# Performance work log

Hardware: AMD Instinct MI355X
Metric: run time of the kernel (lower is better)

## Reference

```python
import jax, jax.numpy as jnp
import numpy as np

B, T, N = 16, 512, 128
D, HID, S, H, L, EMB = 256, 128, 16, 512, 4, 512
EPS_BN = 1e-5
EPS_LN = 1e-5


def _ln(x, w, b):
    mu = x.mean(-1, keepdims=True)
    v = ((x - mu) ** 2).mean(-1, keepdims=True)
    return (x - mu) * jax.lax.rsqrt(v + EPS_LN) * w + b


def _bn(x, w, b):
    # x: (M, N, C); training-mode BatchNorm1d over (batch, spatial), biased var
    mu = x.mean((0, 1))
    v = x.var((0, 1))
    return (x - mu) * jax.lax.rsqrt(v + EPS_BN) * w + b


def setup_inputs() -> dict:
    key = jax.random.key(0)
    ks = iter(jax.random.split(key, 40))
    r = lambda *s: jax.random.normal(next(ks), s, jnp.float32) * 0.05
    inp = dict(
        x=jax.random.normal(next(ks), (B, T, N, 3), jnp.float32),
        lengths=jax.random.randint(next(ks), (B,), 0, T),
        conv1_w=r(HID, 3), bn1_w=1.0 + r(HID), bn1_b=r(HID),
        conv2_w=r(HID, HID), bn2_w=1.0 + r(HID), bn2_b=r(HID),
        fproj_w=r(D, HID), fproj_b=r(D),
        pre_ln_w=1.0 + r(D), pre_ln_b=r(D),
        in_w=r(L, 2 * H, D), in_b=r(L, 2 * H),
        conv_w=r(L, H, 1, 4), conv_b=r(L, H),
        A=r(L, H, S), Bm=r(L, H, S),
        out_w=r(L, D, H), out_b=r(L, D),
        post_ln_w=1.0 + r(D), post_ln_b=r(D),
        m1_w=r(1024, D), m1_b=r(1024),
        m2_w=r(1024, 1024), m2_b=r(1024),
        m3_w=r(EMB, 1024), m3_b=r(EMB),
    )
    return inp


def reference(x, lengths, conv1_w, bn1_w, bn1_b, conv2_w, bn2_w, bn2_b,
              fproj_w, fproj_b, pre_ln_w, pre_ln_b,
              in_w, in_b, conv_w, conv_b, A, Bm, out_w, out_b,
              post_ln_w, post_ln_b, m1_w, m1_b, m2_w, m2_b, m3_w, m3_b):
    Bb, Tt, Nn, _ = x.shape
    xf = x.reshape(Bb * Tt, Nn, 3)
    mu = xf.mean(1, keepdims=True)
    sd = jnp.std(xf, axis=1, ddof=1, keepdims=True) + 1e-10  # torch.std unbiased
    xn = (xf - mu) / sd

    # PointNet frame encoder (1x1 convs == per-point matmuls)
    h1 = jax.nn.relu(_bn(xn @ conv1_w.T, bn1_w, bn1_b))      # (BT, N, HID)
    h2 = jax.nn.relu(_bn(h1 @ conv2_w.T, bn2_w, bn2_b))
    feat = h2.max(1) @ fproj_w.T + fproj_b                   # (BT, D)

    seq = _ln(feat.reshape(Bb, Tt, D), pre_ln_w, pre_ln_b)
    mask = (jnp.arange(Tt)[None, :] < lengths[:, None]).astype(seq.dtype)  # (B, T)
    mk = mask[:, :, None]

    def mamba(seq, iw, ib, cw, cb, Ai, Bi, ow, ob):
        inp = seq @ iw.T + ib                                # (B, T, 2H)
        Hh = inp.shape[-1] // 2
        gate = jax.nn.sigmoid(inp[..., :Hh])
        upd = jax.nn.silu(inp[..., Hh:])
        u = jax.lax.conv_general_dilated(
            upd.transpose(0, 2, 1), cw, (1,), [(2, 2)],
            feature_group_count=Hh, dimension_numbers=('NCH', 'OIH', 'NCH'))
        u = (u + cb[:, None])[:, :, :seq.shape[1]].transpose(0, 2, 1)  # drop extra step
        # masked linear state scan == masked cumulative sum
        Bu = jnp.einsum('bth,hs->bts', u, Bi) * mk           # (B, T, S)
        hstate = jnp.cumsum(Bu, axis=1)
        out = jnp.einsum('bts,hs->bth', hstate, Ai) * gate * mk
        return out @ ow.T + ob

    for i in range(L):
        seq = mamba(seq, in_w[i], in_b[i], conv_w[i], conv_b[i], A[i], Bm[i], out_w[i], out_b[i])

    seq = _ln(seq, post_ln_w, post_ln_b)
    denom = jnp.maximum(lengths, 1).astype(seq.dtype)[:, None]
    pooled = (seq * mk).sum(1) / denom

    e = jax.nn.gelu(pooled @ m1_w.T + m1_b, approximate=False)
    e = jax.nn.gelu(e @ m2_w.T + m2_b, approximate=False)
    e = e @ m3_w.T + m3_b
    return e / jnp.maximum(jnp.linalg.norm(e, axis=1, keepdims=True), 1e-12)
```

## Files before the change

kernel.cpp:

```cpp
#include <hip/hip_runtime.h>
#include <hip/hip_bf16.h>
#include <math.h>

#define NFRM 8192
#define NPT  128
#define CH   128
#define DD   256
#define HH   512
#define SS   16
#define NL   4

typedef __attribute__((ext_vector_type(8))) short bf16x8;
typedef __attribute__((ext_vector_type(4))) float f32x4;
typedef unsigned short u16;

#define MFMA16 __builtin_amdgcn_mfma_f32_16x16x32_bf16


__device__ __forceinline__ float red256(float v, int tid, volatile float* sc) {
#pragma unroll
  for (int off = 32; off; off >>= 1) v += __shfl_down(v, off);
  __syncthreads();
  if ((tid & 63) == 0) sc[tid >> 6] = v;
  __syncthreads();
  return sc[0] + sc[1] + sc[2] + sc[3];
}

__device__ __forceinline__ float sigmoidf_(float x) { return 1.f / (1.f + __expf(-x)); }
__device__ __forceinline__ float geluf_(float x) { return 0.5f * x * (1.f + erff(x * 0.70710678118654752f)); }

__device__ __forceinline__ u16 f2bf(float f) {
  __hip_bfloat16 h = __float2bfloat16(f);
  return *(u16*)&h;
}
__device__ __forceinline__ float bf2f(u16 u) {
  union { unsigned int i; float f; } v; v.i = ((unsigned int)u) << 16; return v.f;
}


__global__ __launch_bounds__(256) void k_prep(const float* __restrict__ conv2_w,
    const float* __restrict__ fproj_w, const float* __restrict__ in_w, const float* __restrict__ out_w,
    const float* __restrict__ A, const float* __restrict__ Bm,
    const float* __restrict__ cw, const float* __restrict__ cb,
    u16* __restrict__ W2B, u16* __restrict__ fprojB, u16* __restrict__ inwB,
    u16* __restrict__ outwB, u16* __restrict__ albB, u16* __restrict__ BmTd,
    float* __restrict__ cbB) {
  int idx = blockIdx.x * 256 + threadIdx.x;
  if (idx < 16384) {
    int c = idx >> 7, k = idx & 127;
    int dst = c * 128 + ((((k >> 3) ^ (c & 7)) << 3) | (k & 7));
    W2B[dst] = f2bf(conv2_w[idx]);
    return;
  }
  idx -= 16384;
  if (idx < 8192) {
    float4 v = ((const float4*)fproj_w)[idx];
    ushort4 o; o.x = f2bf(v.x); o.y = f2bf(v.y); o.z = f2bf(v.z); o.w = f2bf(v.w);
    ((ushort4*)fprojB)[idx] = o;
    return;
  }
  idx -= 8192;
  if (idx < 262144) {
    float4 v = ((const float4*)in_w)[idx];
    ushort4 o; o.x = f2bf(v.x); o.y = f2bf(v.y); o.z = f2bf(v.z); o.w = f2bf(v.w);
    ((ushort4*)inwB)[idx] = o;
    return;
  }
  idx -= 262144;
  if (idx < 131072) {
    float4 v = ((const float4*)out_w)[idx];
    ushort4 o; o.x = f2bf(v.x); o.y = f2bf(v.y); o.z = f2bf(v.z); o.w = f2bf(v.w);
    ((ushort4*)outwB)[idx] = o;
    return;
  }
  idx -= 131072;
  if (idx < 65536) {
    int l = idx >> 14, rem = idx & 16383, h = rem >> 5, kk = rem & 31;
    albB[idx] = (kk < 16) ? f2bf(A[(size_t)l * 8192 + h * 16 + kk]) : (u16)0;
    return;
  }
  idx -= 65536;
  if (idx < 131072) {
    int l = idx >> 15, rem = idx & 32767;
    int d = rem >> 13, rem2 = rem & 8191, s = rem2 >> 9, h = rem2 & 511;
    BmTd[idx] = f2bf(cw[(size_t)l * 2048 + h * 4 + d] * Bm[(size_t)l * 8192 + h * 16 + s]);
    return;
  }
  idx -= 131072;
  if (idx < 4096) {
    int wsl = idx >> 6, lane = idx & 63;
    int l = wsl >> 4, s = wsl & 15;
    float acc = 0.f;
    for (int h = lane; h < 512; h += 64)
      acc = fmaf(cb[l * 512 + h], Bm[(size_t)l * 8192 + h * 16 + s], acc);
#pragma unroll
    for (int off = 32; off; off >>= 1) acc += __shfl_down(acc, off);
    if (lane == 0) cbB[wsl] = acc;
  }
}

__global__ __launch_bounds__(256) void k_mom(const float* __restrict__ x, float* __restrict__ msd,
                                             float* __restrict__ pstat) {
  __shared__ float mpart[4][6];
  int tid = threadIdx.x, lane = tid & 63, w = tid >> 6;
  int f = blockIdx.x * 4 + w;
  const float* xf = x + (size_t)f * 384 + lane * 6;
  float a0 = xf[0], a1 = xf[1], a2 = xf[2], b0 = xf[3], b1 = xf[4], b2 = xf[5];
  float s0 = a0 + b0, s1 = a1 + b1, s2 = a2 + b2;
  float p00 = a0*a0 + b0*b0, p01 = a0*a1 + b0*b1, p02 = a0*a2 + b0*b2;
  float p11 = a1*a1 + b1*b1, p12 = a1*a2 + b1*b2, p22 = a2*a2 + b2*b2;
#pragma unroll
  for (int off = 32; off; off >>= 1) {
    s0 += __shfl_down(s0, off); s1 += __shfl_down(s1, off); s2 += __shfl_down(s2, off);
    p00 += __shfl_down(p00, off); p01 += __shfl_down(p01, off); p02 += __shfl_down(p02, off);
    p11 += __shfl_down(p11, off); p12 += __shfl_down(p12, off); p22 += __shfl_down(p22, off);
  }
  if (lane == 0) {
    float mu0 = s0 * (1.f/128.f), mu1 = s1 * (1.f/128.f), mu2 = s2 * (1.f/128.f);
    float C00 = p00 - 128.f*mu0*mu0, C01 = p01 - 128.f*mu0*mu1, C02 = p02 - 128.f*mu0*mu2;
    float C11 = p11 - 128.f*mu1*mu1, C12 = p12 - 128.f*mu1*mu2, C22 = p22 - 128.f*mu2*mu2;
    float sd0 = sqrtf(C00 * (1.f/127.f)) + 1e-10f;
    float sd1 = sqrtf(C11 * (1.f/127.f)) + 1e-10f;
    float sd2 = sqrtf(C22 * (1.f/127.f)) + 1e-10f;
    mpart[w][0] = C00/(sd0*sd0); mpart[w][1] = C01/(sd0*sd1); mpart[w][2] = C02/(sd0*sd2);
    mpart[w][3] = C11/(sd1*sd1); mpart[w][4] = C12/(sd1*sd2); mpart[w][5] = C22/(sd2*sd2);
    float* d = msd + (size_t)f * 8;
    d[0] = mu0; d[1] = mu1; d[2] = mu2; d[3] = 0.f;
    d[4] = 1.f/sd0; d[5] = 1.f/sd1; d[6] = 1.f/sd2; d[7] = 0.f;
  }
  __syncthreads();
  if (tid < 8) {
    float tot = 0.f;
    if (tid < 6) { for (int w2 = 0; w2 < 4; ++w2) tot += mpart[w2][tid]; }
    pstat[blockIdx.x * 8 + tid] = tot;
  }
}

__global__ __launch_bounds__(256) void k_stats2(const float* __restrict__ pstat, const float* __restrict__ w1,
    const float* __restrict__ bw, const float* __restrict__ bb, float* __restrict__ cc) {
  __shared__ float part[32][8];
  __shared__ float Mt[8];
  int tid = threadIdx.x, j = tid & 7, g = tid >> 3;
  float sm = 0.f;
  for (int r = g; r < 2048; r += 32) sm += pstat[r * 8 + j];
  part[g][j] = sm;
  __syncthreads();
  if (tid < 8) { float tot = 0.f; for (int g2 = 0; g2 < 32; ++g2) tot += part[g2][tid]; Mt[tid] = tot; }
  __syncthreads();
  if (tid < 128) {
    float w0 = w1[tid*3], wa = w1[tid*3+1], wb = w1[tid*3+2];
    float var = (w0*w0*Mt[0] + wa*wa*Mt[3] + wb*wb*Mt[5]
               + 2.f*(w0*wa*Mt[1] + w0*wb*Mt[2] + wa*wb*Mt[4])) * (1.f/1048576.f);
    float s = bw[tid] / sqrtf(var + 1e-5f);
    ((float4*)cc)[tid] = make_float4(s*w0, s*wa, s*wb, bb[tid]);
  }
}

__global__ __launch_bounds__(256) void k2_main(const float* __restrict__ x, const float4* __restrict__ cc,
    const float4* __restrict__ msd4, const u16* __restrict__ W2B,
    float* __restrict__ z2mx, float* __restrict__ z2mn,
    float* __restrict__ psum, float* __restrict__ psq) {
  __shared__ alignas(16) u16 w2s[16384];
  __shared__ float4 ccs[144];
  __shared__ float smx[2][4][CH], smn[2][4][CH], ssm[2][4][CH], ssq[2][4][CH];
  int tid = threadIdx.x;
  for (int i = tid; i < 2048; i += 256) ((float4*)w2s)[i] = ((const float4*)W2B)[i];
  if (tid < 128) ccs[tid + (tid >> 3)] = cc[tid];
  int lane = tid & 63, w = tid >> 6;
  int lr = lane & 15, kg = lane >> 4;
  int row0 = w * 32 + lr, row1 = row0 + 16;
  int f0i = blockIdx.x * 8;
  float4 mu4 = msd4[f0i * 2], rs4 = msd4[f0i * 2 + 1];
  const float* xr0 = x + (size_t)f0i * 384 + row0 * 3;
  const float* xr1 = x + (size_t)f0i * 384 + row1 * 3;
  float cx0 = xr0[0], cx1 = xr0[1], cx2 = xr0[2];
  float cx3 = xr1[0], cx4 = xr1[1], cx5 = xr1[2];
  __syncthreads();
  for (int fi = 0; fi < 8; ++fi) {
    int f = blockIdx.x * 8 + fi;
    int p = fi & 1;
    float xa0 = (cx0 - mu4.x) * rs4.x, xa1 = (cx1 - mu4.y) * rs4.y, xa2 = (cx2 - mu4.z) * rs4.z;
    float xb0 = (cx3 - mu4.x) * rs4.x, xb1 = (cx4 - mu4.y) * rs4.y, xb2 = (cx5 - mu4.z) * rs4.z;
    int fn = (f + 1 < NFRM) ? f + 1 : f;
    float4 nmu = msd4[fn * 2], nrs = msd4[fn * 2 + 1];
    const float* nr0 = x + (size_t)fn * 384 + row0 * 3;
    const float* nr1 = x + (size_t)fn * 384 + row1 * 3;
    float nx0 = nr0[0], nx1 = nr0[1], nx2 = nr0[2];
    float nx3 = nr1[0], nx4 = nr1[1], nx5 = nr1[2];
    f32x4 acc[2][8];
#pragma unroll
    for (int fr = 0; fr < 2; ++fr)
#pragma unroll
      for (int fc = 0; fc < 8; ++fc) acc[fr][fc] = (f32x4){0.f, 0.f, 0.f, 0.f};
#pragma unroll
    for (int ks = 0; ks < 4; ++ks) {
      int kc = ks * 4 + kg;
      int base9 = kc * 9;
      bf16x8 a0, a1;
#pragma unroll
      for (int q = 0; q < 8; ++q) {
        float4 c4 = ccs[base9 + q];
        float h0 = fmaxf(0.f, fmaf(xa0, c4.x, fmaf(xa1, c4.y, fmaf(xa2, c4.z, c4.w))));
        float h1 = fmaxf(0.f, fmaf(xb0, c4.x, fmaf(xb1, c4.y, fmaf(xb2, c4.z, c4.w))));
        a0[q] = (short)f2bf(h0); a1[q] = (short)f2bf(h1);
      }
#pragma unroll
      for (int fc = 0; fc < 8; ++fc) {
        int col = fc * 16 + lr;
        bf16x8 b = *(const bf16x8*)&w2s[col * 128 + ((kc ^ (col & 7)) << 3)];
        acc[0][fc] = MFMA16(a0, b, acc[0][fc], 0, 0, 0);
        acc[1][fc] = MFMA16(a1, b, acc[1][fc], 0, 0, 0);
      }
    }
#pragma unroll
    for (int fc = 0; fc < 8; ++fc) {
      float mx = -3e38f, mn = 3e38f, sm = 0.f, sq = 0.f;
#pragma unroll
      for (int fr = 0; fr < 2; ++fr)
#pragma unroll
        for (int r = 0; r < 4; ++r) {
          float v = acc[fr][fc][r];
          mx = fmaxf(mx, v); mn = fminf(mn, v); sm += v; sq = fmaf(v, v, sq);
        }
#pragma unroll
      for (int off = 16; off <= 32; off <<= 1) {
        mx = fmaxf(mx, __shfl_xor(mx, off));
        mn = fminf(mn, __shfl_xor(mn, off));
        sm += __shfl_xor(sm, off);
        sq += __shfl_xor(sq, off);
      }
      if (lane < 16) {
        int col = fc * 16 + lr;
        smx[p][w][col] = mx; smn[p][w][col] = mn; ssm[p][w][col] = sm; ssq[p][w][col] = sq;
      }
    }
    __syncthreads();
    if (tid < CH) {
      float mx = smx[p][0][tid], mn = smn[p][0][tid], sm = ssm[p][0][tid], sq = ssq[p][0][tid];
#pragma unroll
      for (int w2 = 1; w2 < 4; ++w2) {
        mx = fmaxf(mx, smx[p][w2][tid]); mn = fminf(mn, smn[p][w2][tid]);
        sm += ssm[p][w2][tid]; sq += ssq[p][w2][tid];
      }
      z2mx[(size_t)f * CH + tid] = mx;
      z2mn[(size_t)f * CH + tid] = mn;
      psum[(size_t)f * CH + tid] = sm;
      psq[(size_t)f * CH + tid]  = sq;
    }
    cx0 = nx0; cx1 = nx1; cx2 = nx2; cx3 = nx3; cx4 = nx4; cx5 = nx5;
    mu4 = nmu; rs4 = nrs;
  }
}

__global__ __launch_bounds__(256) void k_red1(const float* __restrict__ psum, const float* __restrict__ psq,
    float* __restrict__ prs, float* __restrict__ prq) {
  __shared__ float s0[2][128], s1[2][128];
  int tid = threadIdx.x, c = tid & 127, half = tid >> 7;
  int f0 = blockIdx.x * 128;
  float sm = 0.f, sq = 0.f;
  for (int fl = half; fl < 128; fl += 2) {
    size_t idx = (size_t)(f0 + fl) * 128 + c;
    sm += psum[idx]; sq += psq[idx];
  }
  s0[half][c] = sm; s1[half][c] = sq;
  __syncthreads();
  if (tid < 128) {
    prs[blockIdx.x * 128 + tid] = s0[0][tid] + s0[1][tid];
    prq[blockIdx.x * 128 + tid] = s1[0][tid] + s1[1][tid];
  }
}

__global__ __launch_bounds__(256) void k_red2(const float* __restrict__ prs, const float* __restrict__ prq,
    const float* __restrict__ w, const float* __restrict__ b, float* __restrict__ st,
    float invM, float eps) {
  __shared__ float s0[2][128], s1[2][128];
  int tid = threadIdx.x, c = tid & 127, half = tid >> 7;
  float sm = 0.f, sq = 0.f;
  for (int g = half; g < 64; g += 2) { sm += prs[g * 128 + c]; sq += prq[g * 128 + c]; }
  s0[half][c] = sm; s1[half][c] = sq;
  __syncthreads();
  if (tid < 128) {
    float tsm = s0[0][tid] + s0[1][tid], tsq = s1[0][tid] + s1[1][tid];
    float mean = tsm * invM;
    float var = tsq * invM - mean * mean;
    float s = w[tid] / sqrtf(var + eps);
    st[tid] = s;
    st[CH + tid] = b[tid] - mean * s;
  }
}

__global__ __launch_bounds__(512) void k_fi(const float* __restrict__ z2mx, const float* __restrict__ z2mn,
    const float* __restrict__ s2t2, const u16* __restrict__ fprojB, const float* __restrict__ fpb,
    const float* __restrict__ plw, const float* __restrict__ plb,
    const u16* __restrict__ inwB_l, const float* __restrict__ inb,
    u16* __restrict__ gate, u16* __restrict__ upd) {
  __shared__ alignas(16) u16 h2s[32 * 128];
  __shared__ float ft[32 * 260];
  __shared__ alignas(16) u16 as[32 * 256];
  int f0 = blockIdx.x * 32, tid = threadIdx.x;
  int lane = tid & 63, w = tid >> 6, lr = lane & 15, kg = lane >> 4;
  {
    int row = tid >> 4, cc = tid & 15, c0 = cc * 8;
    const float* zx = z2mx + (size_t)(f0 + row) * 128 + c0;
    const float* zn = z2mn + (size_t)(f0 + row) * 128 + c0;
    bf16x8 v;
#pragma unroll
    for (int q = 0; q < 8; ++q) {
      int c = c0 + q;
      float s = s2t2[c], t = s2t2[128 + c];
      float z = (s >= 0.f) ? zx[q] : zn[q];
      v[q] = (short)f2bf(fmaxf(0.f, fmaf(s, z, t)));
    }
    *(bf16x8*)&h2s[row * 128 + ((cc ^ (row & 7)) << 3)] = v;
  }
  __syncthreads();
  {
    f32x4 fac[2][2];
#pragma unroll
    for (int fr = 0; fr < 2; ++fr)
#pragma unroll
      for (int fc = 0; fc < 2; ++fc) fac[fr][fc] = (f32x4){0.f, 0.f, 0.f, 0.f};
#pragma unroll
    for (int ks = 0; ks < 4; ++ks) {
      int kc = ks * 4 + kg;
      bf16x8 a0 = *(const bf16x8*)&h2s[lr * 128 + ((kc ^ (lr & 7)) << 3)];
      bf16x8 a1 = *(const bf16x8*)&h2s[(16 + lr) * 128 + ((kc ^ (lr & 7)) << 3)];
#pragma unroll
      for (int fc = 0; fc < 2; ++fc) {
        int d = w * 32 + fc * 16 + lr;
        bf16x8 b = *(const bf16x8*)&fprojB[(size_t)d * 128 + kc * 8];
        fac[0][fc] = MFMA16(a0, b, fac[0][fc], 0, 0, 0);
        fac[1][fc] = MFMA16(a1, b, fac[1][fc], 0, 0, 0);
      }
    }
#pragma unroll
    for (int fr = 0; fr < 2; ++fr)
#pragma unroll
      for (int fc = 0; fc < 2; ++fc) {
        int d = w * 32 + fc * 16 + lr;
        float bias = fpb[d];
#pragma unroll
        for (int r = 0; r < 4; ++r) {
          int row = fr * 16 + kg * 4 + r;
          ft[row * 260 + d] = fac[fr][fc][r] + bias;
        }
      }
  }
  __syncthreads();
  {
    float4 plw4 = ((const float4*)plw)[lane];
    float4 plb4 = ((const float4*)plb)[lane];
#pragma unroll
    for (int q = 0; q < 4; ++q) {
      int row = w * 4 + q;
      float4 v = *(const float4*)&ft[row * 260 + lane * 4];
      float s = v.x + v.y + v.z + v.w;
#pragma unroll
      for (int off = 32; off; off >>= 1) s += __shfl_xor(s, off);
      float mu = s * (1.f / 256.f);
      float4 dd = make_float4(v.x - mu, v.y - mu, v.z - mu, v.w - mu);
      float qq = dd.x*dd.x + dd.y*dd.y + dd.z*dd.z + dd.w*dd.w;
#pragma unroll
      for (int off = 32; off; off >>= 1) qq += __shfl_xor(qq, off);
      float rs = 1.f / sqrtf(qq * (1.f / 256.f) + 1e-5f);
      u16 o[4];
      o[0] = f2bf(fmaf(dd.x * rs, plw4.x, plb4.x));
      o[1] = f2bf(fmaf(dd.y * rs, plw4.y, plb4.y));
      o[2] = f2bf(fmaf(dd.z * rs, plw4.z, plb4.z));
      o[3] = f2bf(fmaf(dd.w * rs, plw4.w, plb4.w));
      int chunk = lane >> 1;
      *(uint2*)&as[row * 256 + ((chunk ^ (row & 7)) << 3) + (lane & 1) * 4] = *(uint2*)o;
    }
  }
  __syncthreads();
  f32x4 acc[2][8];
#pragma unroll
  for (int fr = 0; fr < 2; ++fr)
#pragma unroll
    for (int fc = 0; fc < 8; ++fc) acc[fr][fc] = (f32x4){0.f, 0.f, 0.f, 0.f};
  int colb = w * 128;
#pragma unroll
  for (int ks = 0; ks < 8; ++ks) {
    int kc = ks * 4 + kg;
    int r1 = 16 + lr;
    bf16x8 a0 = *(const bf16x8*)&as[lr * 256 + ((kc ^ (lr & 7)) << 3)];
    bf16x8 a1 = *(const bf16x8*)&as[r1 * 256 + ((kc ^ (r1 & 7)) << 3)];
#pragma unroll
    for (int fc = 0; fc < 8; ++fc) {
      int col = colb + fc * 16 + lr;
      bf16x8 b = *(const bf16x8*)&inwB_l[(size_t)col * 256 + kc * 8];
      acc[0][fc] = MFMA16(a0, b, acc[0][fc], 0, 0, 0);
      acc[1][fc] = MFMA16(a1, b, acc[1][fc], 0, 0, 0);
    }
  }
  bool isGate = (w < 4);
  u16* dst = isGate ? gate : upd;
  int cbOff = isGate ? 0 : 512;
#pragma unroll
  for (int fr = 0; fr < 2; ++fr)
#pragma unroll
    for (int fc = 0; fc < 8; ++fc) {
      int cg = colb + fc * 16 + lr;
      float bias = inb[cg];
      int colOut = cg - cbOff;
#pragma unroll
      for (int r = 0; r < 4; ++r) {
        int frame = f0 + fr * 16 + kg * 4 + r;
        float v = acc[fr][fc][r] + bias;
        float sg = sigmoidf_(v);
        v = isGate ? sg : v * sg;
        dst[(size_t)frame * 512 + colOut] = f2bf(v);
      }
    }
}

__global__ __launch_bounds__(256) void k_bu(const u16* __restrict__ updB, const u16* __restrict__ BmTd_l,
    const float* __restrict__ cbB_l, const int* __restrict__ lengths, float* __restrict__ bu) {
  __shared__ float part[2][32][16];
  int tid = threadIdx.x, lane = tid & 63, w = tid >> 6;
  int wf = w & 1, hh = w >> 1;
  int f0 = blockIdx.x * 32 + wf * 16;
  int lr = lane & 15, kg = lane >> 4;
  int t = (f0 & 511) + lr;
  const u16* arow = updB + (size_t)(f0 + lr) * 512;
  bool v0 = (t >= 2), v1 = (t >= 1), v3 = (t <= 510);
  const bf16x8 zv = (bf16x8){0,0,0,0,0,0,0,0};
  f32x4 acc = (f32x4){0.f, 0.f, 0.f, 0.f};
#pragma unroll
  for (int ks = 0; ks < 8; ++ks) {
    int kc = hh * 32 + ks * 4 + kg, co = kc * 8;
    bf16x8 a0 = v0 ? *(const bf16x8*)&arow[co - 1024] : zv;
    bf16x8 a1 = v1 ? *(const bf16x8*)&arow[co - 512]  : zv;
    bf16x8 a2 =      *(const bf16x8*)&arow[co];
    bf16x8 a3 = v3 ? *(const bf16x8*)&arow[co + 512]  : zv;
    acc = MFMA16(a0, *(const bf16x8*)&BmTd_l[0 * 8192 + lr * 512 + co], acc, 0, 0, 0);
    acc = MFMA16(a1, *(const bf16x8*)&BmTd_l[1 * 8192 + lr * 512 + co], acc, 0, 0, 0);
    acc = MFMA16(a2, *(const bf16x8*)&BmTd_l[2 * 8192 + lr * 512 + co], acc, 0, 0, 0);
    acc = MFMA16(a3, *(const bf16x8*)&BmTd_l[3 * 8192 + lr * 512 + co], acc, 0, 0, 0);
  }
#pragma unroll
  for (int r = 0; r < 4; ++r) part[hh][wf * 16 + kg * 4 + r][lr] = acc[r];
  __syncthreads();
  int len = lengths[blockIdx.x >> 4];
  for (int i = tid; i < 512; i += 256) {
    int fl = i >> 4, s = i & 15;
    int frame = blockIdx.x * 32 + fl;
    int tt = frame & 511, bi = frame >> 9;
    float val = part[0][fl][s] + part[1][fl][s] + cbB_l[s];
    bu[((size_t)bi * 16 + s) * 512 + tt] = (tt < len) ? val : 0.f;
  }
}

__global__ __launch_bounds__(512) void k_mo(const float* __restrict__ bu,
    u16* __restrict__ gateB, u16* __restrict__ updB,
    const u16* __restrict__ albB_l, const u16* __restrict__ outwB_l, const float* __restrict__ outb,
    const u16* __restrict__ inwB_n, const float* __restrict__ inb_n,
    const int* __restrict__ lengths) {
  __shared__ alignas(16) u16 hsb[32 * 40];
  __shared__ alignas(16) u16 vl[32 * 512];
  __shared__ alignas(16) u16 as[32 * 256];
  int f0 = blockIdx.x * 32, tid = threadIdx.x;
  int bb = f0 >> 9, tbase = f0 & 511;
  int len = lengths[bb];
  int lane = tid & 63, w = tid >> 6, lr = lane & 15, kg = lane >> 4;
  for (int i = tid; i < 640; i += 512) ((unsigned int*)hsb)[i] = 0;
  __syncthreads();
#pragma unroll
  for (int q = 0; q < 2; ++q) {
    int s = w * 2 + q;
    const float* src = bu + ((size_t)bb * 16 + s) * 512 + lane * 8;
    float4 v0 = *(const float4*)src, v1 = *(const float4*)(src + 4);
    float p0 = v0.x, p1 = p0 + v0.y, p2 = p1 + v0.z, p3 = p2 + v0.w;
    float p4 = p3 + v1.x, p5 = p4 + v1.y, p6 = p5 + v1.z, p7 = p6 + v1.w;
    float tot = p7;
#pragma unroll
    for (int off = 1; off < 64; off <<= 1) {
      float n = __shfl_up(tot, off);
      if (lane >= off) tot += n;
    }
    float excl = tot - p7;
    int rbase = lane * 8 - tbase;
    if (rbase >= 0 && rbase < 32) {
      hsb[(rbase + 0) * 40 + s] = f2bf(p0 + excl);
      hsb[(rbase + 1) * 40 + s] = f2bf(p1 + excl);
      hsb[(rbase + 2) * 40 + s] = f2bf(p2 + excl);
      hsb[(rbase + 3) * 40 + s] = f2bf(p3 + excl);
      hsb[(rbase + 4) * 40 + s] = f2bf(p4 + excl);
      hsb[(rbase + 5) * 40 + s] = f2bf(p5 + excl);
      hsb[(rbase + 6) * 40 + s] = f2bf(p6 + excl);
      hsb[(rbase + 7) * 40 + s] = f2bf(p7 + excl);
    }
  }
  __syncthreads();
  {
    bf16x8 a0 = *(const bf16x8*)&hsb[lr * 40 + kg * 8];
    bf16x8 a1 = *(const bf16x8*)&hsb[(16 + lr) * 40 + kg * 8];
    f32x4 zero = (f32x4){0.f, 0.f, 0.f, 0.f};
#pragma unroll
    for (int fc = 0; fc < 4; ++fc) {
      int h = w * 64 + fc * 16 + lr;
      bf16x8 b = *(const bf16x8*)&albB_l[h * 32 + kg * 8];
      f32x4 va = MFMA16(a0, b, zero, 0, 0, 0);
      f32x4 vb = MFMA16(a1, b, zero, 0, 0, 0);
      int hck = h >> 3, hlo = h & 7;
#pragma unroll
      for (int fr = 0; fr < 2; ++fr) {
        f32x4 vv = fr ? vb : va;
#pragma unroll
        for (int r = 0; r < 4; ++r) {
          int fl = fr * 16 + kg * 4 + r;
          int frame = f0 + fl;
          float g = bf2f(gateB[(size_t)frame * 512 + h]);
          float val = ((frame & 511) < len) ? vv[r] * g : 0.f;
          vl[fl * 512 + ((hck ^ (fl & 7)) << 3) + hlo] = f2bf(val);
        }
      }
    }
  }
  __syncthreads();
  {
    f32x4 acc2[2][2];
#pragma unroll
    for (int fr = 0; fr < 2; ++fr)
#pragma unroll
      for (int fc = 0; fc < 2; ++fc) acc2[fr][fc] = (f32x4){0.f, 0.f, 0.f, 0.f};
    int db = w * 32;
#pragma unroll
    for (int ks = 0; ks < 16; ++ks) {
      int kc = ks * 4 + kg;
      int r1 = 16 + lr;
      bf16x8 a0 = *(const bf16x8*)&vl[lr * 512 + ((kc ^ (lr & 7)) << 3)];
      bf16x8 a1 = *(const bf16x8*)&vl[r1 * 512 + ((kc ^ (r1 & 7)) << 3)];
#pragma unroll
      for (int fc = 0; fc < 2; ++fc) {
        int d = db + fc * 16 + lr;
        bf16x8 b = *(const bf16x8*)&outwB_l[(size_t)d * 512 + kc * 8];
        acc2[0][fc] = MFMA16(a0, b, acc2[0][fc], 0, 0, 0);
        acc2[1][fc] = MFMA16(a1, b, acc2[1][fc], 0, 0, 0);
      }
    }
#pragma unroll
    for (int fr = 0; fr < 2; ++fr)
#pragma unroll
      for (int fc = 0; fc < 2; ++fc) {
        int d = db + fc * 16 + lr;
        float bias = outb[d];
        int dck = d >> 3, dlo = d & 7;
#pragma unroll
        for (int r = 0; r < 4; ++r) {
          int row = fr * 16 + kg * 4 + r;
          as[row * 256 + ((dck ^ (row & 7)) << 3) + dlo] = f2bf(acc2[fr][fc][r] + bias);
        }
      }
  }
  __syncthreads();
  f32x4 acc[2][8];
#pragma unroll
  for (int fr = 0; fr < 2; ++fr)
#pragma unroll
    for (int fc = 0; fc < 8; ++fc) acc[fr][fc] = (f32x4){0.f, 0.f, 0.f, 0.f};
  int colb = w * 128;
#pragma unroll
  for (int ks = 0; ks < 8; ++ks) {
    int kc = ks * 4 + kg;
    int r1 = 16 + lr;
    bf16x8 a0 = *(const bf16x8*)&as[lr * 256 + ((kc ^ (lr & 7)) << 3)];
    bf16x8 a1 = *(const bf16x8*)&as[r1 * 256 + ((kc ^ (r1 & 7)) << 3)];
#pragma unroll
    for (int fc = 0; fc < 8; ++fc) {
      int col = colb + fc * 16 + lr;
      bf16x8 b = *(const bf16x8*)&inwB_n[(size_t)col * 256 + kc * 8];
      acc[0][fc] = MFMA16(a0, b, acc[0][fc], 0, 0, 0);
      acc[1][fc] = MFMA16(a1, b, acc[1][fc], 0, 0, 0);
    }
  }
  bool isGate = (w < 4);
  u16* dst = isGate ? gateB : updB;
  int cbOff = isGate ? 0 : 512;
#pragma unroll
  for (int fr = 0; fr < 2; ++fr)
#pragma unroll
    for (int fc = 0; fc < 8; ++fc) {
      int cg = colb + fc * 16 + lr;
      float bias = inb_n[cg];
      int colOut = cg - cbOff;
#pragma unroll
      for (int r = 0; r < 4; ++r) {
        int frame = f0 + fr * 16 + kg * 4 + r;
        float v = acc[fr][fc][r] + bias;
        float sg = sigmoidf_(v);
        v = isGate ? sg : v * sg;
        dst[(size_t)frame * 512 + colOut] = f2bf(v);
      }
    }
}

__global__ __launch_bounds__(256) void k_out(const float* __restrict__ bu, const u16* __restrict__ gateB,
    const u16* __restrict__ albB_l, const u16* __restrict__ outwB_l, const float* __restrict__ outb,
    const int* __restrict__ lengths, float* __restrict__ sout) {
  __shared__ alignas(16) u16 hsb[32 * 40];
  __shared__ alignas(16) u16 vl[32 * 512];
  int f0 = blockIdx.x * 32, tid = threadIdx.x;
  int bb = f0 >> 9, tbase = f0 & 511;
  int len = lengths[bb];
  int lane = tid & 63, w = tid >> 6, lr = lane & 15, kg = lane >> 4;
  for (int i = tid; i < 640; i += 256) ((unsigned int*)hsb)[i] = 0;
  __syncthreads();
#pragma unroll
  for (int q = 0; q < 4; ++q) {
    int s = w * 4 + q;
    const float* src = bu + ((size_t)bb * 16 + s) * 512 + lane * 8;
    float4 v0 = *(const float4*)src, v1 = *(const float4*)(src + 4);
    float p0 = v0.x, p1 = p0 + v0.y, p2 = p1 + v0.z, p3 = p2 + v0.w;
    float p4 = p3 + v1.x, p5 = p4 + v1.y, p6 = p5 + v1.z, p7 = p6 + v1.w;
    float tot = p7;
#pragma unroll
    for (int off = 1; off < 64; off <<= 1) {
      float n = __shfl_up(tot, off);
      if (lane >= off) tot += n;
    }
    float excl = tot - p7;
    int rbase = lane * 8 - tbase;
    if (rbase >= 0 && rbase < 32) {
      hsb[(rbase + 0) * 40 + s] = f2bf(p0 + excl);
      hsb[(rbase + 1) * 40 + s] = f2bf(p1 + excl);
      hsb[(rbase + 2) * 40 + s] = f2bf(p2 + excl);
      hsb[(rbase + 3) * 40 + s] = f2bf(p3 + excl);
      hsb[(rbase + 4) * 40 + s] = f2bf(p4 + excl);
      hsb[(rbase + 5) * 40 + s] = f2bf(p5 + excl);
      hsb[(rbase + 6) * 40 + s] = f2bf(p6 + excl);
      hsb[(rbase + 7) * 40 + s] = f2bf(p7 + excl);
    }
  }
  __syncthreads();
  {
    bf16x8 a0 = *(const bf16x8*)&hsb[lr * 40 + kg * 8];
    bf16x8 a1 = *(const bf16x8*)&hsb[(16 + lr) * 40 + kg * 8];
    f32x4 zero = (f32x4){0.f, 0.f, 0.f, 0.f};
#pragma unroll
    for (int fc = 0; fc < 8; ++fc) {
      int h = w * 128 + fc * 16 + lr;
      bf16x8 b = *(const bf16x8*)&albB_l[h * 32 + kg * 8];
      f32x4 va = MFMA16(a0, b, zero, 0, 0, 0);
      f32x4 vb = MFMA16(a1, b, zero, 0, 0, 0);
      int hck = h >> 3, hlo = h & 7;
#pragma unroll
      for (int fr = 0; fr < 2; ++fr) {
        f32x4 vv = fr ? vb : va;
#pragma unroll
        for (int r = 0; r < 4; ++r) {
          int fl = fr * 16 + kg * 4 + r;
          int frame = f0 + fl;
          float g = bf2f(gateB[(size_t)frame * 512 + h]);
          float val = ((frame & 511) < len) ? vv[r] * g : 0.f;
          vl[fl * 512 + ((hck ^ (fl & 7)) << 3) + hlo] = f2bf(val);
        }
      }
    }
  }
  __syncthreads();
  f32x4 acc[2][4];
#pragma unroll
  for (int fr = 0; fr < 2; ++fr)
#pragma unroll
    for (int fc = 0; fc < 4; ++fc) acc[fr][fc] = (f32x4){0.f, 0.f, 0.f, 0.f};
  int db = w * 64;
#pragma unroll
  for (int ks = 0; ks < 16; ++ks) {
    int kc = ks * 4 + kg;
    int r1 = 16 + lr;
    bf16x8 a0 = *(const bf16x8*)&vl[lr * 512 + ((kc ^ (lr & 7)) << 3)];
    bf16x8 a1 = *(const bf16x8*)&vl[r1 * 512 + ((kc ^ (r1 & 7)) << 3)];
#pragma unroll
    for (int fc = 0; fc < 4; ++fc) {
      int d = db + fc * 16 + lr;
      bf16x8 b = *(const bf16x8*)&outwB_l[(size_t)d * 512 + kc * 8];
      acc[0][fc] = MFMA16(a0, b, acc[0][fc], 0, 0, 0);
      acc[1][fc] = MFMA16(a1, b, acc[1][fc], 0, 0, 0);
    }
  }
#pragma unroll
  for (int fr = 0; fr < 2; ++fr)
#pragma unroll
    for (int fc = 0; fc < 4; ++fc) {
      int d = db + fc * 16 + lr;
      float bias = outb[d];
#pragma unroll
      for (int r = 0; r < 4; ++r) {
        int frame = f0 + fr * 16 + kg * 4 + r;
        sout[(size_t)frame * 256 + d] = acc[fr][fc][r] + bias;
      }
    }
}

__global__ __launch_bounds__(512) void k_pp1(const float* __restrict__ seq, const int* __restrict__ lengths,
    const float* __restrict__ w, const float* __restrict__ b, float* __restrict__ ppart) {
  __shared__ float4 part[8][64];
  int bb = blockIdx.x >> 3, ck = blockIdx.x & 7;
  int tid = threadIdx.x, lane = tid & 63, wv = tid >> 6;
  int len = lengths[bb];
  float4 w4 = ((const float4*)w)[lane], b4 = ((const float4*)b)[lane];
  float4 pacc = make_float4(0.f, 0.f, 0.f, 0.f);
#pragma unroll
  for (int it = 0; it < 8; ++it) {
    int t = ck * 64 + it * 8 + wv;
    float4 v = ((const float4*)(seq + ((size_t)bb * 512 + t) * DD))[lane];
    float s = v.x + v.y + v.z + v.w;
#pragma unroll
    for (int off = 32; off; off >>= 1) s += __shfl_xor(s, off);
    float mu = s * (1.f / 256.f);
    float4 dd = make_float4(v.x - mu, v.y - mu, v.z - mu, v.w - mu);
    float q = dd.x*dd.x + dd.y*dd.y + dd.z*dd.z + dd.w*dd.w;
#pragma unroll
    for (int off = 32; off; off >>= 1) q += __shfl_xor(q, off);
    float rs = 1.f / sqrtf(q * (1.f / 256.f) + 1e-5f);
    if (t < len) {
      pacc.x += fmaf(dd.x * rs, w4.x, b4.x);
      pacc.y += fmaf(dd.y * rs, w4.y, b4.y);
      pacc.z += fmaf(dd.z * rs, w4.z, b4.z);
      pacc.w += fmaf(dd.w * rs, w4.w, b4.w);
    }
  }
  part[wv][lane] = pacc;
  __syncthreads();
  if (tid < 64) {
    float4 a = part[0][tid];
#pragma unroll
    for (int w2 = 1; w2 < 8; ++w2) {
      float4 p = part[w2][tid];
      a.x += p.x; a.y += p.y; a.z += p.z; a.w += p.w;
    }
    ((float4*)(ppart + (size_t)blockIdx.x * DD))[tid] = a;
  }
}

__global__ __launch_bounds__(256) void k_pp2(const float* __restrict__ ppart, const int* __restrict__ lengths,
    float* __restrict__ pooled) {
  int bb = blockIdx.x, d = threadIdx.x;
  float a = 0.f;
#pragma unroll
  for (int ck = 0; ck < 8; ++ck) a += ppart[(size_t)(bb * 8 + ck) * DD + d];
  pooled[(size_t)bb * DD + d] = a / (float)max(lengths[bb], 1);
}

__global__ __launch_bounds__(256) void k_mlp(const float* __restrict__ in, const float* __restrict__ W,
    const float* __restrict__ bias, float* __restrict__ out, int K, int Nout, int act) {
  __shared__ float lin[16 * 1024];
  int tid = threadIdx.x, lane = tid & 63, w = tid >> 6;
  for (int i = tid; i < 16 * K / 4; i += 256) ((float4*)lin)[i] = ((const float4*)in)[i];
  __syncthreads();
  int o = blockIdx.x * 4 + w;
  const float4* wr4 = (const float4*)(W + (size_t)o * K);
  float acc[16];
#pragma unroll
  for (int r = 0; r < 16; ++r) acc[r] = 0.f;
  for (int k4 = lane; k4 < K / 4; k4 += 64) {
    float4 wv = wr4[k4];
    int kb = k4 * 4;
#pragma unroll
    for (int r = 0; r < 16; ++r) {
      float4 lv = *(const float4*)&lin[r * K + kb];
      acc[r] = fmaf(lv.x, wv.x, fmaf(lv.y, wv.y, fmaf(lv.z, wv.z, fmaf(lv.w, wv.w, acc[r]))));
    }
  }
#pragma unroll
  for (int r = 0; r < 16; ++r) {
#pragma unroll
    for (int off = 32; off; off >>= 1) acc[r] += __shfl_xor(acc[r], off);
  }
  if (lane < 16) {
    float v = 0.f;
#pragma unroll
    for (int r = 0; r < 16; ++r) if (lane == r) v = acc[r];
    v += bias[o];
    if (act) v = geluf_(v);
    out[(size_t)lane * Nout + o] = v;
  }
}

__global__ __launch_bounds__(256) void k_norm(const float* __restrict__ e, float* __restrict__ out) {
  __shared__ float sc[4];
  int b = blockIdx.x, tid = threadIdx.x;
  float v0 = e[(size_t)b * 512 + tid], v1 = e[(size_t)b * 512 + 256 + tid];
  float ss = red256(v0 * v0 + v1 * v1, tid, sc);
  float nrm = fmaxf(sqrtf(ss), 1e-12f);
  out[(size_t)b * 512 + tid] = v0 / nrm;
  out[(size_t)b * 512 + 256 + tid] = v1 / nrm;
}


extern "C" void kernel_launch(void* const* d_in, const int* in_sizes, int n_in,
                              void* d_out, int out_size, void* d_ws, size_t ws_size,
                              hipStream_t stream) {
  const float* x         = (const float*)d_in[0];
  const int*   lengths   = (const int*)d_in[1];
  const float* conv1_w   = (const float*)d_in[2];
  const float* bn1_w     = (const float*)d_in[3];
  const float* bn1_b     = (const float*)d_in[4];
  const float* conv2_w   = (const float*)d_in[5];
  const float* bn2_w     = (const float*)d_in[6];
  const float* bn2_b     = (const float*)d_in[7];
  const float* fproj_w   = (const float*)d_in[8];
  const float* fproj_b   = (const float*)d_in[9];
  const float* pre_ln_w  = (const float*)d_in[10];
  const float* pre_ln_b  = (const float*)d_in[11];
  const float* in_w      = (const float*)d_in[12];
  const float* in_b      = (const float*)d_in[13];
  const float* conv_w    = (const float*)d_in[14];
  const float* conv_b    = (const float*)d_in[15];
  const float* A         = (const float*)d_in[16];
  const float* Bm        = (const float*)d_in[17];
  const float* out_w     = (const float*)d_in[18];
  const float* out_b     = (const float*)d_in[19];
  const float* post_ln_w = (const float*)d_in[20];
  const float* post_ln_b = (const float*)d_in[21];
  const float* m1_w      = (const float*)d_in[22];
  const float* m1_b      = (const float*)d_in[23];
  const float* m2_w      = (const float*)d_in[24];
  const float* m2_b      = (const float*)d_in[25];
  const float* m3_w      = (const float*)d_in[26];
  const float* m3_b      = (const float*)d_in[27];
  float* outp = (float*)d_out;

  float* wsf = (float*)d_ws;
  size_t o = 0;
  auto F32 = [&](size_t n) { float* p = wsf + o; o += (n + 63) & ~(size_t)63; return p; };
  float* psum   = F32(1048576);
  float* psq    = F32(1048576);
  float* z2mx   = F32(1048576);
  float* z2mn   = F32(1048576);
  float* msd    = F32(65536);
  float* pstat  = F32(16384);
  float* cc     = F32(512);
  float* s2t2   = F32(256);
  float* prs    = F32(8192);
  float* prq    = F32(8192);
  u16*   W2B    = (u16*)F32(8192);
  u16*   fprojB = (u16*)F32(16384);
  u16*   inwB   = (u16*)F32(524288);
  u16*   outwB  = (u16*)F32(262144);
  u16*   albB   = (u16*)F32(32768);
  u16*   BmTd   = (u16*)F32(65536);
  float* cbB    = F32(64);
  float* seqA   = F32(2097152);
  u16*   gateB  = (u16*)F32(2097152);
  u16*   updB   = (u16*)F32(2097152);
  float* buv    = F32(131072);
  float* ppart  = F32(32768);
  float* pooled = F32(4096);
  float* e1     = F32(16384);
  float* e2     = F32(16384);
  float* e3     = F32(8192);
  if (ws_size < o * sizeof(float)) return;

  const float invM = 1.f / (float)(NFRM * NPT);

  k_prep<<<2416, 256, 0, stream>>>(conv2_w, fproj_w, in_w, out_w, A, Bm, conv_w, conv_b,
                                   W2B, fprojB, inwB, outwB, albB, BmTd, cbB);
  k_mom<<<2048, 256, 0, stream>>>(x, msd, pstat);
  k_stats2<<<1, 256, 0, stream>>>(pstat, conv1_w, bn1_w, bn1_b, cc);
  k2_main<<<NFRM / 8, 256, 0, stream>>>(x, (const float4*)cc, (const float4*)msd, W2B,
                                        z2mx, z2mn, psum, psq);
  k_red1<<<64, 256, 0, stream>>>(psum, psq, prs, prq);
  k_red2<<<1, 256, 0, stream>>>(prs, prq, bn2_w, bn2_b, s2t2, invM, 1e-5f);
  k_fi<<<NFRM / 32, 512, 0, stream>>>(z2mx, z2mn, s2t2, fprojB, fproj_b, pre_ln_w, pre_ln_b,
                                      inwB, in_b, gateB, updB);

  for (int l = 0; l < 3; ++l) {
    k_bu<<<NFRM / 32, 256, 0, stream>>>(updB, BmTd + (size_t)l * 32768, cbB + l * 16, lengths, buv);
    k_mo<<<NFRM / 32, 512, 0, stream>>>(buv, gateB, updB,
                                        albB + (size_t)l * 16384, outwB + (size_t)l * 131072,
                                        out_b + l * 256,
                                        inwB + (size_t)(l + 1) * 262144, in_b + (l + 1) * 1024,
                                        lengths);
  }
  k_bu<<<NFRM / 32, 256, 0, stream>>>(updB, BmTd + (size_t)3 * 32768, cbB + 3 * 16, lengths, buv);
  k_out<<<NFRM / 32, 256, 0, stream>>>(buv, gateB, albB + (size_t)3 * 16384,
                                       outwB + (size_t)3 * 131072, out_b + 3 * 256, lengths, seqA);
  k_pp1<<<128, 512, 0, stream>>>(seqA, lengths, post_ln_w, post_ln_b, ppart);
  k_pp2<<<16, 256, 0, stream>>>(ppart, lengths, pooled);
  k_mlp<<<256, 256, 0, stream>>>(pooled, m1_w, m1_b, e1, 256, 1024, 1);
  k_mlp<<<256, 256, 0, stream>>>(e1, m2_w, m2_b, e2, 1024, 1024, 1);
  k_mlp<<<128, 256, 0, stream>>>(e2, m3_w, m3_b, e3, 1024, 512, 0);
  k_norm<<<16, 256, 0, stream>>>(e3, outp);
}
```

Baseline: 405.7 us.

## Fuse tail reductions via last-block atomics and halve frames per k2_main block

Folds the single-block BN1 stats kernel into k_mom and the BN2 second-stage reduction into k_red, using a threadfence plus atomic counter so the last finishing block does the final reduction. Folds the pooling kernel k_pp2 into the first MLP kernel's input load. Also changes k2_main to 4 frames per block with twice as many blocks. The aim is fewer kernel launches and tiny serial single-block kernels, in exchange for a counter memset, atomics, and more redundant W2 loads into LDS in k2_main.

After: 522.8 us. 28.8% more time.

```diff
diff --git a/kernel.cpp b/kernel.cpp
--- a/kernel.cpp
+++ b/kernel.cpp
@@ -100,8 +100,12 @@
 }
 
 __global__ __launch_bounds__(256) void k_mom(const float* __restrict__ x, float* __restrict__ msd,
-                                             float* __restrict__ pstat) {
+    float* __restrict__ pstat, const float* __restrict__ w1, const float* __restrict__ bw,
+    const float* __restrict__ bb, float* __restrict__ cc, unsigned int* __restrict__ cnt) {
   __shared__ float mpart[4][6];
+  __shared__ float part2[32][8];
+  __shared__ float Mt[8];
+  __shared__ unsigned int lastv;
   int tid = threadIdx.x, lane = tid & 63, w = tid >> 6;
   int f = blockIdx.x * 4 + w;
   const float* xf = x + (size_t)f * 384 + lane * 6;
@@ -134,25 +138,26 @@
     if (tid < 6) { for (int w2 = 0; w2 < 4; ++w2) tot += mpart[w2][tid]; }
     pstat[blockIdx.x * 8 + tid] = tot;
   }
-}
-
-__global__ __launch_bounds__(256) void k_stats2(const float* __restrict__ pstat, const float* __restrict__ w1,
-    const float* __restrict__ bw, const float* __restrict__ bb, float* __restrict__ cc) {
-  __shared__ float part[32][8];
-  __shared__ float Mt[8];
-  int tid = threadIdx.x, j = tid & 7, g = tid >> 3;
-  float sm = 0.f;
-  for (int r = g; r < 2048; r += 32) sm += pstat[r * 8 + j];
-  part[g][j] = sm;
-  __syncthreads();
-  if (tid < 8) { float tot = 0.f; for (int g2 = 0; g2 < 32; ++g2) tot += part[g2][tid]; Mt[tid] = tot; }
-  __syncthreads();
-  if (tid < 128) {
-    float w0 = w1[tid*3], wa = w1[tid*3+1], wb = w1[tid*3+2];
-    float var = (w0*w0*Mt[0] + wa*wa*Mt[3] + wb*wb*Mt[5]
-               + 2.f*(w0*wa*Mt[1] + w0*wb*Mt[2] + wa*wb*Mt[4])) * (1.f/1048576.f);
-    float s = bw[tid] / sqrtf(var + 1e-5f);
-    ((float4*)cc)[tid] = make_float4(s*w0, s*wa, s*wb, bb[tid]);
+  __threadfence();
+  __syncthreads();
+  if (tid == 0) lastv = atomicAdd(cnt, 1u);
+  __syncthreads();
+  if (lastv != gridDim.x - 1) return;
+  {
+    int j = tid & 7, g = tid >> 3;
+    float sm = 0.f;
+    for (int r = g; r < 2048; r += 32) sm += pstat[r * 8 + j];
+    part2[g][j] = sm;
+    __syncthreads();
+    if (tid < 8) { float tot = 0.f; for (int g2 = 0; g2 < 32; ++g2) tot += part2[g2][tid]; Mt[tid] = tot; }
+    __syncthreads();
+    if (tid < 128) {
+      float w0 = w1[tid*3], wa = w1[tid*3+1], wb = w1[tid*3+2];
+      float var = (w0*w0*Mt[0] + wa*wa*Mt[3] + wb*wb*Mt[5]
+                 + 2.f*(w0*wa*Mt[1] + w0*wb*Mt[2] + wa*wb*Mt[4])) * (1.f/1048576.f);
+      float s = bw[tid] / sqrtf(var + 1e-5f);
+      ((float4*)cc)[tid] = make_float4(s*w0, s*wa, s*wb, bb[tid]);
+    }
   }
 }
 
@@ -169,15 +174,15 @@
   int lane = tid & 63, w = tid >> 6;
   int lr = lane & 15, kg = lane >> 4;
   int row0 = w * 32 + lr, row1 = row0 + 16;
-  int f0i = blockIdx.x * 8;
+  int f0i = blockIdx.x * 4;
   float4 mu4 = msd4[f0i * 2], rs4 = msd4[f0i * 2 + 1];
   const float* xr0 = x + (size_t)f0i * 384 + row0 * 3;
   const float* xr1 = x + (size_t)f0i * 384 + row1 * 3;
   float cx0 = xr0[0], cx1 = xr0[1], cx2 = xr0[2];
   float cx3 = xr1[0], cx4 = xr1[1], cx5 = xr1[2];
   __syncthreads();
-  for (int fi = 0; fi < 8; ++fi) {
-    int f = blockIdx.x * 8 + fi;
+  for (int fi = 0; fi < 4; ++fi) {
+    int f = blockIdx.x * 4 + fi;
     int p = fi & 1;
     float xa0 = (cx0 - mu4.x) * rs4.x, xa1 = (cx1 - mu4.y) * rs4.y, xa2 = (cx2 - mu4.z) * rs4.z;
     float xb0 = (cx3 - mu4.x) * rs4.x, xb1 = (cx4 - mu4.y) * rs4.y, xb2 = (cx5 - mu4.z) * rs4.z;
@@ -252,9 +257,12 @@
   }
 }
 
-__global__ __launch_bounds__(256) void k_red1(const float* __restrict__ psum, const float* __restrict__ psq,
-    float* __restrict__ prs, float* __restrict__ prq) {
+__global__ __launch_bounds__(256) void k_red(const float* __restrict__ psum, const float* __restrict__ psq,
+    const float* __restrict__ w, const float* __restrict__ b, float* __restrict__ st,
+    float* __restrict__ prs, float* __restrict__ prq, unsigned int* __restrict__ cnt,
+    float invM, float eps) {
   __shared__ float s0[2][128], s1[2][128];
+  __shared__ unsigned int lastv;
   int tid = threadIdx.x, c = tid & 127, half = tid >> 7;
   int f0 = blockIdx.x * 128;
   float sm = 0.f, sq = 0.f;
@@ -268,15 +276,14 @@
     prs[blockIdx.x * 128 + tid] = s0[0][tid] + s0[1][tid];
     prq[blockIdx.x * 128 + tid] = s1[0][tid] + s1[1][tid];
   }
-}
-
-__global__ __launch_bounds__(256) void k_red2(const float* __restrict__ prs, const float* __restrict__ prq,
-    const float* __restrict__ w, const float* __restrict__ b, float* __restrict__ st,
-    float invM, float eps) {
-  __shared__ float s0[2][128], s1[2][128];
-  int tid = threadIdx.x, c = tid & 127, half = tid >> 7;
-  float sm = 0.f, sq = 0.f;
+  __threadfence();
+  __syncthreads();
+  if (tid == 0) lastv = atomicAdd(cnt, 1u);
+  __syncthreads();
+  if (lastv != gridDim.x - 1) return;
+  sm = 0.f; sq = 0.f;
   for (int g = half; g < 64; g += 2) { sm += prs[g * 128 + c]; sq += prq[g * 128 + c]; }
+  __syncthreads();
   s0[half][c] = sm; s1[half][c] = sq;
   __syncthreads();
   if (tid < 128) {
@@ -734,20 +741,22 @@
   }
 }
 
-__global__ __launch_bounds__(256) void k_pp2(const float* __restrict__ ppart, const int* __restrict__ lengths,
-    float* __restrict__ pooled) {
-  int bb = blockIdx.x, d = threadIdx.x;
-  float a = 0.f;
-#pragma unroll
-  for (int ck = 0; ck < 8; ++ck) a += ppart[(size_t)(bb * 8 + ck) * DD + d];
-  pooled[(size_t)bb * DD + d] = a / (float)max(lengths[bb], 1);
-}
-
 __global__ __launch_bounds__(256) void k_mlp(const float* __restrict__ in, const float* __restrict__ W,
-    const float* __restrict__ bias, float* __restrict__ out, int K, int Nout, int act) {
+    const float* __restrict__ bias, float* __restrict__ out, int K, int Nout, int act,
+    const int* __restrict__ lengths, int mode) {
   __shared__ float lin[16 * 1024];
   int tid = threadIdx.x, lane = tid & 63, w = tid >> 6;
-  for (int i = tid; i < 16 * K / 4; i += 256) ((float4*)lin)[i] = ((const float4*)in)[i];
+  if (mode) {
+    for (int i = tid; i < 16 * 256; i += 256) {
+      int r = i >> 8, c2 = i & 255;
+      float a = 0.f;
+#pragma unroll
+      for (int ck = 0; ck < 8; ++ck) a += in[(size_t)((r << 3) + ck) * 256 + c2];
+      lin[r * 256 + c2] = a / (float)max(lengths[r], 1);
+    }
+  } else {
+    for (int i = tid; i < 16 * K / 4; i += 256) ((float4*)lin)[i] = ((const float4*)in)[i];
+  }
   __syncthreads();
   int o = blockIdx.x * 4 + w;
   const float4* wr4 = (const float4*)(W + (size_t)o * K);
@@ -835,6 +844,7 @@
   float* s2t2   = F32(256);
   float* prs    = F32(8192);
   float* prq    = F32(8192);
+  float* cnts   = F32(64);
   u16*   W2B    = (u16*)F32(8192);
   u16*   fprojB = (u16*)F32(16384);
   u16*   inwB   = (u16*)F32(524288);
@@ -847,7 +857,6 @@
   u16*   updB   = (u16*)F32(2097152);
   float* buv    = F32(131072);
   float* ppart  = F32(32768);
-  float* pooled = F32(4096);
   float* e1     = F32(16384);
   float* e2     = F32(16384);
   float* e3     = F32(8192);
@@ -855,14 +864,15 @@
 
   const float invM = 1.f / (float)(NFRM * NPT);
 
+  hipMemsetAsync(cnts, 0, 8, stream);
   k_prep<<<2416, 256, 0, stream>>>(conv2_w, fproj_w, in_w, out_w, A, Bm, conv_w, conv_b,
                                    W2B, fprojB, inwB, outwB, albB, BmTd, cbB);
-  k_mom<<<2048, 256, 0, stream>>>(x, msd, pstat);
-  k_stats2<<<1, 256, 0, stream>>>(pstat, conv1_w, bn1_w, bn1_b, cc);
-  k2_main<<<NFRM / 8, 256, 0, stream>>>(x, (const float4*)cc, (const float4*)msd, W2B,
+  k_mom<<<2048, 256, 0, stream>>>(x, msd, pstat, conv1_w, bn1_w, bn1_b, cc,
+                                  (unsigned int*)cnts);
+  k2_main<<<NFRM / 4, 256, 0, stream>>>(x, (const float4*)cc, (const float4*)msd, W2B,
                                         z2mx, z2mn, psum, psq);
-  k_red1<<<64, 256, 0, stream>>>(psum, psq, prs, prq);
-  k_red2<<<1, 256, 0, stream>>>(prs, prq, bn2_w, bn2_b, s2t2, invM, 1e-5f);
+  k_red<<<64, 256, 0, stream>>>(psum, psq, bn2_w, bn2_b, s2t2, prs, prq,
+                                (unsigned int*)cnts + 1, invM, 1e-5f);
   k_fi<<<NFRM / 32, 512, 0, stream>>>(z2mx, z2mn, s2t2, fprojB, fproj_b, pre_ln_w, pre_ln_b,
                                       inwB, in_b, gateB, updB);
 
@@ -878,9 +888,8 @@
   k_out<<<NFRM / 32, 256, 0, stream>>>(buv, gateB, albB + (size_t)3 * 16384,
                                        outwB + (size_t)3 * 131072, out_b + 3 * 256, lengths, seqA);
   k_pp1<<<128, 512, 0, stream>>>(seqA, lengths, post_ln_w, post_ln_b, ppart);
-  k_pp2<<<16, 256, 0, stream>>>(ppart, lengths, pooled);
-  k_mlp<<<256, 256, 0, stream>>>(pooled, m1_w, m1_b, e1, 256, 1024, 1);
-  k_mlp<<<256, 256, 0, stream>>>(e1, m2_w, m2_b, e2, 1024, 1024, 1);
-  k_mlp<<<128, 256, 0, stream>>>(e2, m3_w, m3_b, e3, 1024, 512, 0);
+  k_mlp<<<256, 256, 0, stream>>>(ppart, m1_w, m1_b, e1, 256, 1024, 1, lengths, 1);
+  k_mlp<<<256, 256, 0, stream>>>(e1, m2_w, m2_b, e2, 1024, 1024, 1, lengths, 0);
+  k_mlp<<<128, 256, 0, stream>>>(e2, m3_w, m3_b, e3, 1024, 512, 0, lengths, 0);
   k_norm<<<16, 256, 0, stream>>>(e3, outp);
 }
```
